# Kernel tuning notes

Measured on AMD Instinct MI355X. Metric: run time of the kernel, lower is better.

## Reference

```python
import jax, jax.numpy as jnp
import numpy as np

N, S, I, L, M = 4096, 8, 256, 512, 256


def setup_inputs() -> dict:
    key = jax.random.key(0)
    ks = jax.random.split(key, 13)
    sc_in = 1.0 / np.sqrt(I + L)
    sc_out = 1.0 / np.sqrt(L)
    return {
        "modulation": jax.random.normal(ks[0], (N, S * I), jnp.float32),
        "h0": jax.random.normal(ks[1], (N, S * L), jnp.float32),
        "c0": jax.random.normal(ks[2], (N, S * L), jnp.float32),
        "Wi": jax.random.normal(ks[3], (S, L, I + L), jnp.float32) * sc_in,
        "bi": jnp.full((S, L), -1.0, jnp.float32),  # init_input bias
        "Wf": jax.random.normal(ks[4], (S, L, I + L), jnp.float32) * sc_in,
        "bf": jnp.full((S, L), 1.0, jnp.float32),   # init_forget bias
        "Wg": jax.random.normal(ks[5], (S, L, I + L), jnp.float32) * sc_in,
        "bg": jnp.zeros((S, L), jnp.float32),
        "Wo": jax.random.normal(ks[6], (S, L, I + L), jnp.float32) * sc_in,
        "bo": jnp.zeros((S, L), jnp.float32),
        "Wy": jax.random.normal(ks[7], (S, M, L), jnp.float32) * sc_out,
        "by": jnp.zeros((S, M), jnp.float32),
    }


def reference(modulation, h0, c0, Wi, bi, Wf, bf, Wg, bg, Wo, bo, Wy, by):
    n = modulation.shape[0]
    x = modulation.reshape(n, S, I)          # [N,S,I]
    h = h0.reshape(n, S, L)                  # [N,S,L]
    c = c0.reshape(n, S, L)
    xh = jnp.concatenate([x, h], axis=-1)    # cat_groups: per-stream [x_s, h_s] -> [N,S,I+L]
    # grouped per-stream linear projections for the four gates
    i = jax.nn.sigmoid(jnp.einsum('nsd,sld->nsl', xh, Wi) + bi)
    f = jax.nn.sigmoid(jnp.einsum('nsd,sld->nsl', xh, Wf) + bf)
    g = jnp.tanh(jnp.einsum('nsd,sld->nsl', xh, Wg) + bg)
    o = jax.nn.sigmoid(jnp.einsum('nsd,sld->nsl', xh, Wo) + bo)
    c_new = f * c + i * g
    h_new = o * jnp.tanh(c_new)              # dropout p=0 -> identity
    y = jnp.einsum('nsl,sml->nsm', h_new, Wy) + by
    return y.reshape(n, S * M)
```

## Files before the change

### kernel.cpp

```cpp
#include <hip/hip_runtime.h>
#include <stdint.h>

#define S_ 8
#define N_ 4096
#define I_ 256
#define L_ 512
#define M_ 256
#define D_ 768
#define NT64 12

typedef __bf16 bf16x8 __attribute__((ext_vector_type(8)));
typedef float f32x4 __attribute__((ext_vector_type(4)));
typedef unsigned short ushort_t;

__device__ __forceinline__ unsigned short f2bf(float f) {
  union { float f; uint32_t u; } c; c.f = f;
  uint32_t u = c.u;
  uint32_t r = u + 0x7FFFu + ((u >> 16) & 1u);
  return (unsigned short)(r >> 16);
}

__device__ __forceinline__ float fsigmoid(float x) {
  return 1.0f / (1.0f + __expf(-x));
}
__device__ __forceinline__ float ftanh(float x) {
  float ax = fabsf(x);
  float e = __expf(-2.0f * ax);
  float t = (1.0f - e) / (1.0f + e);
  return copysignf(t, x);
}

#define GLD16(gsrc, ldst)                                                                  \
  __builtin_amdgcn_global_load_lds(                                                        \
      (const __attribute__((address_space(1))) uint32_t*)(uintptr_t)(gsrc),                \
      (__attribute__((address_space(3))) uint32_t*)(uintptr_t)(ldst), 16, 0, 0)

__global__ __launch_bounds__(256) void prep_kernel(
    const float* __restrict__ mod, const float* __restrict__ h0,
    const float* __restrict__ Wi, const float* __restrict__ Wf,
    const float* __restrict__ Wg, const float* __restrict__ Wo,
    const float* __restrict__ Wy, ushort_t* __restrict__ w4,
    ushort_t* __restrict__ wyb, ushort_t* __restrict__ xh) {
  const int y = blockIdx.y;
  int t = blockIdx.x * 256 + threadIdx.x;
  const int stride = gridDim.x * 256;
  if (y < 4) {
    const float* src = (y == 0) ? Wi : (y == 1) ? Wf : (y == 2) ? Wg : Wo;
    ushort_t* dst = w4 + (size_t)y * S_ * L_ * D_;
    const int n4 = S_ * L_ * D_ / 4;
    for (; t < n4; t += stride) {
      float4 v = ((const float4*)src)[t];
      ushort4 o;
      o.x = f2bf(v.x); o.y = f2bf(v.y); o.z = f2bf(v.z); o.w = f2bf(v.w);
      ((ushort4*)dst)[t] = o;
    }
  } else if (y == 4) {
    const int n4 = S_ * M_ * L_ / 4;
    for (; t < n4; t += stride) {
      float4 v = ((const float4*)Wy)[t];
      ushort4 o;
      o.x = f2bf(v.x); o.y = f2bf(v.y); o.z = f2bf(v.z); o.w = f2bf(v.w);
      ((ushort4*)wyb)[t] = o;
    }
  } else if (y == 5) {
    const int total = S_ * N_ * (I_ / 4);
    for (; t < total; t += stride) {
      int r = t >> 6, c = t & 63;
      int s = r >> 12, n = r & (N_ - 1);
      float4 v = *(const float4*)(mod + (size_t)n * (S_ * I_) + s * I_ + c * 4);
      ushort4 o;
      o.x = f2bf(v.x); o.y = f2bf(v.y); o.z = f2bf(v.z); o.w = f2bf(v.w);
      *(ushort4*)(xh + (size_t)r * D_ + c * 4) = o;
    }
  } else {
    const int total = S_ * N_ * (L_ / 4);
    for (; t < total; t += stride) {
      int r = t >> 7, c = t & 127;
      int s = r >> 12, n = r & (N_ - 1);
      float4 v = *(const float4*)(h0 + (size_t)n * (S_ * L_) + s * L_ + c * 4);
      ushort4 o;
      o.x = f2bf(v.x); o.y = f2bf(v.y); o.z = f2bf(v.z); o.w = f2bf(v.w);
      *(ushort4*)(xh + (size_t)r * D_ + I_ + c * 4) = o;
    }
  }
}

__global__ __launch_bounds__(1024, 4) void gates_kernel(
    const ushort_t* __restrict__ xh,
    const ushort_t* __restrict__ w4,
    const float* __restrict__ bi, const float* __restrict__ bff,
    const float* __restrict__ bg, const float* __restrict__ bo,
    const float* __restrict__ c0,
    ushort_t* __restrict__ hout)
{
  __shared__ __align__(16) ushort_t smem[65536];
  const int tid = threadIdx.x;
  const int lane = tid & 63;
  const int ln15 = lane & 15;
  const int ln4 = lane >> 4;
  const int w = tid >> 6;
  const int wm = w >> 2;
  const int wl = w & 3;

  const int bid = blockIdx.x;
  const int s = bid & 7;
  const int r = bid >> 3;
  const int n0 = (r >> 3) << 8;
  const int l0 = (r & 7) << 6;

  const size_t xh_base = (size_t)(s * N_ + n0) * D_;

  const ushort_t* aSrc[2];
  const ushort_t* bSrc[2];
  #pragma unroll
  for (int rd = 0; rd < 2; ++rd) {
    int slot = tid + (rd << 10);
    int row = slot >> 3;
    int cg = (slot & 7) ^ (row & 7);
    aSrc[rd] = xh + xh_base + (size_t)row * D_ + (cg << 3);
    int g = row >> 6, ll = row & 63;
    bSrc[rd] = w4 + ((size_t)((g * S_ + s) * L_) + l0 + ll) * D_ + (cg << 3);
  }

#define STAGE(base, tile) do {                                                          \
    const int k0_ = (tile) << 6;                                                        \
    GLD16(aSrc[0] + k0_, &smem[((base) + (w << 6)) * 8]);                               \
    GLD16(aSrc[1] + k0_, &smem[((base) + 1024 + (w << 6)) * 8]);                        \
    GLD16(bSrc[0] + k0_, &smem[((base) + 2048 + (w << 6)) * 8]);                        \
    GLD16(bSrc[1] + k0_, &smem[((base) + 3072 + (w << 6)) * 8]);                        \
  } while (0)

  f32x4 acc[4][4];
  #pragma unroll
  for (int i = 0; i < 4; ++i)
    #pragma unroll
    for (int j = 0; j < 4; ++j) {
      f32x4 z = {0.f, 0.f, 0.f, 0.f};
      acc[i][j] = z;
    }

  STAGE(0, 0);
  asm volatile("s_waitcnt vmcnt(0)" ::: "memory");
  __syncthreads();

  #pragma unroll 1
  for (int t = 0; t < NT64; ++t) {
    const int cur = (t & 1) << 12;
    if (t + 1 < NT64) STAGE(cur ^ 4096, t + 1);

    #pragma unroll
    for (int kk = 0; kk < 2; ++kk) {
      const int ch = (kk << 2) + ln4;
      bf16x8 a[4];
      #pragma unroll
      for (int rt = 0; rt < 4; ++rt) {
        int ra = (wm << 6) + (rt << 4) + ln15;
        a[rt] = *(const bf16x8*)&smem[(cur + (ra << 3) + (ch ^ (ra & 7))) * 8];
      }
      bf16x8 b[4];
      #pragma unroll
      for (int g = 0; g < 4; ++g) {
        int rB = (g << 6) + (wl << 4) + ln15;
        b[g] = *(const bf16x8*)&smem[(cur + 2048 + (rB << 3) + (ch ^ (rB & 7))) * 8];
      }
      #pragma unroll
      for (int rt = 0; rt < 4; ++rt)
        #pragma unroll
        for (int g = 0; g < 4; ++g)
          acc[rt][g] = __builtin_amdgcn_mfma_f32_16x16x32_bf16(a[rt], b[g], acc[rt][g], 0, 0, 0);
    }

    asm volatile("s_waitcnt vmcnt(0)" ::: "memory");
    __syncthreads();
  }

  const int l = l0 + (wl << 4) + ln15;
  const float vbi = bi[s * L_ + l];
  const float vbf = bff[s * L_ + l];
  const float vbg = bg[s * L_ + l];
  const float vbo = bo[s * L_ + l];
  #pragma unroll
  for (int rt = 0; rt < 4; ++rt) {
    #pragma unroll
    for (int j = 0; j < 4; ++j) {
      const int n = n0 + (wm << 6) + (rt << 4) + (ln4 << 2) + j;
      const float c0v = c0[(size_t)n * (S_ * L_) + s * L_ + l];
      const float iv = fsigmoid(acc[rt][0][j] + vbi);
      const float fv = fsigmoid(acc[rt][1][j] + vbf);
      const float gv = ftanh(acc[rt][2][j] + vbg);
      const float ov = fsigmoid(acc[rt][3][j] + vbo);
      const float cn = fv * c0v + iv * gv;
      const float hn = ov * ftanh(cn);
      hout[(size_t)(s * N_ + n) * L_ + l] = f2bf(hn);
    }
  }
#undef STAGE
}

__global__ __launch_bounds__(256, 2) void out_kernel(
    const ushort_t* __restrict__ h,
    const ushort_t* __restrict__ wy,
    const float* __restrict__ by,
    float* __restrict__ out)
{
  __shared__ __align__(16) ushort_t smem[1536 * 8];
  const int tid = threadIdx.x;
  const int lane = tid & 63;
  const int w = tid >> 6;
  const int n0 = blockIdx.x * 128;
  const int m0 = blockIdx.y * 64;
  const int s = blockIdx.z;

  f32x4 acc[2][4];
  #pragma unroll
  for (int rt = 0; rt < 2; ++rt)
    #pragma unroll
    for (int ct = 0; ct < 4; ++ct) {
      f32x4 z = {0.f, 0.f, 0.f, 0.f};
      acc[rt][ct] = z;
    }

  const size_t h_row0 = (size_t)(s * N_ + n0) * L_;

  for (int t = 0; t < L_ / 64; ++t) {
    const int k0 = t * 64;
    #pragma unroll
    for (int it = 0; it < 4; ++it) {
      int chunk = it * 256 + tid;
      int rr = chunk >> 3, c = chunk & 7;
      int cg = c ^ (rr & 7);
      const ushort_t* src = h + h_row0 + (size_t)rr * L_ + k0 + cg * 8;
      GLD16(src, &smem[(it * 256 + w * 64) * 8]);
    }
    #pragma unroll
    for (int it = 0; it < 2; ++it) {
      int chunk = it * 256 + tid;
      int rl = chunk >> 3, c = chunk & 7;
      int cg = c ^ (rl & 7);
      const ushort_t* src = wy + ((size_t)(s * M_ + m0 + rl)) * L_ + k0 + cg * 8;
      GLD16(src, &smem[(1024 + it * 256 + w * 64) * 8]);
    }
    __syncthreads();
    #pragma unroll
    for (int kk = 0; kk < 2; ++kk) {
      const int cc = kk * 4 + (lane >> 4);
      bf16x8 av[2];
      #pragma unroll
      for (int rt = 0; rt < 2; ++rt) {
        int rr = w * 32 + rt * 16 + (lane & 15);
        av[rt] = *(const bf16x8*)&smem[(rr * 8 + (cc ^ (rr & 7))) * 8];
      }
      #pragma unroll
      for (int ct = 0; ct < 4; ++ct) {
        int rl = ct * 16 + (lane & 15);
        bf16x8 b = *(const bf16x8*)&smem[(1024 + rl * 8 + (cc ^ (rl & 7))) * 8];
        acc[0][ct] = __builtin_amdgcn_mfma_f32_16x16x32_bf16(av[0], b, acc[0][ct], 0, 0, 0);
        acc[1][ct] = __builtin_amdgcn_mfma_f32_16x16x32_bf16(av[1], b, acc[1][ct], 0, 0, 0);
      }
    }
    __syncthreads();
  }

  #pragma unroll
  for (int ct = 0; ct < 4; ++ct) {
    const int m = m0 + ct * 16 + (lane & 15);
    const float vb = by[s * M_ + m];
    #pragma unroll
    for (int rt = 0; rt < 2; ++rt) {
      #pragma unroll
      for (int j = 0; j < 4; ++j) {
        const int n = n0 + w * 32 + rt * 16 + (lane >> 4) * 4 + j;
        out[(size_t)n * (S_ * M_) + s * M_ + m] = acc[rt][ct][j] + vb;
      }
    }
  }
}


extern "C" void kernel_launch(void* const* d_in, const int* in_sizes, int n_in,
                              void* d_out, int out_size, void* d_ws, size_t ws_size,
                              hipStream_t stream) {
  const float* mod = (const float*)d_in[0];
  const float* h0  = (const float*)d_in[1];
  const float* c0  = (const float*)d_in[2];
  const float* Wi  = (const float*)d_in[3];
  const float* bi  = (const float*)d_in[4];
  const float* Wf  = (const float*)d_in[5];
  const float* bf  = (const float*)d_in[6];
  const float* Wg  = (const float*)d_in[7];
  const float* bg  = (const float*)d_in[8];
  const float* Wo  = (const float*)d_in[9];
  const float* bo  = (const float*)d_in[10];
  const float* Wy  = (const float*)d_in[11];
  const float* by  = (const float*)d_in[12];
  float* out = (float*)d_out;

  ushort_t* ws = (ushort_t*)d_ws;
  ushort_t* xh   = ws;
  ushort_t* w4   = xh  + (size_t)S_ * N_ * D_;
  ushort_t* wyb  = w4  + (size_t)4 * S_ * L_ * D_;
  ushort_t* hbuf = wyb + (size_t)S_ * M_ * L_;

  prep_kernel<<<dim3(768, 7), 256, 0, stream>>>(mod, h0, Wi, Wf, Wg, Wo, Wy, w4, wyb, xh);
  gates_kernel<<<1024, 1024, 0, stream>>>(xh, w4, bi, bf, bg, bo, c0, hbuf);
  out_kernel<<<dim3(N_ / 128, M_ / 64, S_), 256, 0, stream>>>(hbuf, wyb, by, out);
}
```

Before: 197.8 us.

## Halve gates block threads, double per-wave tile, software-pipeline LDS reads and prefetch

The gates GEMM block drops from 1024 to 512 threads, so each wave now computes an 8x4 MFMA tile, twice the rows it handled before. Global loads are now prefetched two K-tiles ahead using partial vmcnt waits. The two K-halves of each tile have their LDS fragment reads double-buffered in registers so reads overlap MFMAs. The aim is to cut barrier/sync overhead and LDS traffic per MFMA and to hide global latency better, at the cost of more VGPRs/AGPRs and possibly lower occupancy.

```diff
diff --git a/kernel.cpp b/kernel.cpp
--- a/kernel.cpp
+++ b/kernel.cpp
@@ -85,7 +85,7 @@
   }
 }
 
-__global__ __launch_bounds__(1024, 4) void gates_kernel(
+__global__ __launch_bounds__(512, 2) void gates_kernel(
     const ushort_t* __restrict__ xh,
     const ushort_t* __restrict__ w4,
     const float* __restrict__ bi, const float* __restrict__ bff,
@@ -110,11 +110,11 @@
 
   const size_t xh_base = (size_t)(s * N_ + n0) * D_;
 
-  const ushort_t* aSrc[2];
-  const ushort_t* bSrc[2];
-  #pragma unroll
-  for (int rd = 0; rd < 2; ++rd) {
-    int slot = tid + (rd << 10);
+  const ushort_t* aSrc[4];
+  const ushort_t* bSrc[4];
+  #pragma unroll
+  for (int rd = 0; rd < 4; ++rd) {
+    int slot = tid + (rd << 9);
     int row = slot >> 3;
     int cg = (slot & 7) ^ (row & 7);
     aSrc[rd] = xh + xh_base + (size_t)row * D_ + (cg << 3);
@@ -122,56 +122,82 @@
     bSrc[rd] = w4 + ((size_t)((g * S_ + s) * L_) + l0 + ll) * D_ + (cg << 3);
   }
 
-#define STAGE(base, tile) do {                                                          \
+#define STAGE(bs, tile) do {                                                            \
     const int k0_ = (tile) << 6;                                                        \
-    GLD16(aSrc[0] + k0_, &smem[((base) + (w << 6)) * 8]);                               \
-    GLD16(aSrc[1] + k0_, &smem[((base) + 1024 + (w << 6)) * 8]);                        \
-    GLD16(bSrc[0] + k0_, &smem[((base) + 2048 + (w << 6)) * 8]);                        \
-    GLD16(bSrc[1] + k0_, &smem[((base) + 3072 + (w << 6)) * 8]);                        \
+    _Pragma("unroll")                                                                   \
+    for (int rd_ = 0; rd_ < 4; ++rd_) {                                                 \
+      GLD16(aSrc[rd_] + k0_, &smem[((bs) + (rd_ << 9) + (w << 6)) * 8]);                \
+      GLD16(bSrc[rd_] + k0_, &smem[((bs) + 2048 + (rd_ << 9) + (w << 6)) * 8]);         \
+    }                                                                                   \
   } while (0)
 
-  f32x4 acc[4][4];
-  #pragma unroll
-  for (int i = 0; i < 4; ++i)
+  const char* smemB = (const char*)smem;
+  const uint32_t chk0 = (uint32_t)((ln4 ^ (ln15 & 7)) << 4);
+  const uint32_t chk1 = (uint32_t)(((4 + ln4) ^ (ln15 & 7)) << 4);
+  const uint32_t aBase = (uint32_t)(((wm << 7) + ln15) << 7);
+  const uint32_t bBase = 32768u + (uint32_t)(((wl << 4) + ln15) << 7);
+  const uint32_t aK0 = aBase + chk0, aK1 = aBase + chk1;
+  const uint32_t bK0 = bBase + chk0, bK1 = bBase + chk1;
+
+#define READS(dstA, dstB, aK, bK, bufB) do {                                            \
+    const char* pA_ = smemB + ((aK) + (bufB));                                          \
+    const char* pB_ = smemB + ((bK) + (bufB));                                          \
+    _Pragma("unroll")                                                                   \
+    for (int rt_ = 0; rt_ < 8; ++rt_) dstA[rt_] = *(const bf16x8*)(pA_ + rt_ * 2048);   \
+    _Pragma("unroll")                                                                   \
+    for (int g_ = 0; g_ < 4; ++g_) dstB[g_] = *(const bf16x8*)(pB_ + g_ * 8192);        \
+  } while (0)
+
+#define MFMAS(aset, bset) do {                                                          \
+    _Pragma("unroll")                                                                   \
+    for (int rt_ = 0; rt_ < 8; ++rt_)                                                   \
+      _Pragma("unroll")                                                                 \
+      for (int g_ = 0; g_ < 4; ++g_)                                                    \
+        acc[rt_][g_] = __builtin_amdgcn_mfma_f32_16x16x32_bf16(                         \
+            aset[rt_], bset[g_], acc[rt_][g_], 0, 0, 0);                                \
+  } while (0)
+
+#define LGKM0() asm volatile("s_waitcnt lgkmcnt(0)")
+#define BAR() __builtin_amdgcn_s_barrier()
+
+  f32x4 acc[8][4];
+  #pragma unroll
+  for (int i = 0; i < 8; ++i)
     #pragma unroll
     for (int j = 0; j < 4; ++j) {
       f32x4 z = {0.f, 0.f, 0.f, 0.f};
       acc[i][j] = z;
     }
 
+  bf16x8 a0[8], b0[4], a1[8], b1[4];
+
   STAGE(0, 0);
-  asm volatile("s_waitcnt vmcnt(0)" ::: "memory");
-  __syncthreads();
+  STAGE(4096, 1);
+  asm volatile("s_waitcnt vmcnt(8)" ::: "memory");
+  BAR();
+  READS(a0, b0, aK0, bK0, 0u);
+  LGKM0();
 
   #pragma unroll 1
   for (int t = 0; t < NT64; ++t) {
-    const int cur = (t & 1) << 12;
-    if (t + 1 < NT64) STAGE(cur ^ 4096, t + 1);
-
-    #pragma unroll
-    for (int kk = 0; kk < 2; ++kk) {
-      const int ch = (kk << 2) + ln4;
-      bf16x8 a[4];
-      #pragma unroll
-      for (int rt = 0; rt < 4; ++rt) {
-        int ra = (wm << 6) + (rt << 4) + ln15;
-        a[rt] = *(const bf16x8*)&smem[(cur + (ra << 3) + (ch ^ (ra & 7))) * 8];
-      }
-      bf16x8 b[4];
-      #pragma unroll
-      for (int g = 0; g < 4; ++g) {
-        int rB = (g << 6) + (wl << 4) + ln15;
-        b[g] = *(const bf16x8*)&smem[(cur + 2048 + (rB << 3) + (ch ^ (rB & 7))) * 8];
-      }
-      #pragma unroll
-      for (int rt = 0; rt < 4; ++rt)
-        #pragma unroll
-        for (int g = 0; g < 4; ++g)
-          acc[rt][g] = __builtin_amdgcn_mfma_f32_16x16x32_bf16(a[rt], b[g], acc[rt][g], 0, 0, 0);
-    }
-
-    asm volatile("s_waitcnt vmcnt(0)" ::: "memory");
-    __syncthreads();
+    const uint32_t curB = (uint32_t)(t & 1) << 16;
+    const uint32_t nxtB = curB ^ 65536u;
+    const int bsCur = (t & 1) << 12;
+
+    READS(a1, b1, aK1, bK1, curB);
+    MFMAS(a0, b0);
+    LGKM0();
+    BAR();
+    if (t + 2 < NT64) STAGE(bsCur, t + 2);
+    if (t < NT64 - 2) {
+      asm volatile("s_waitcnt vmcnt(8)" ::: "memory");
+    } else {
+      asm volatile("s_waitcnt vmcnt(0)" ::: "memory");
+    }
+    BAR();
+    if (t + 1 < NT64) READS(a0, b0, aK0, bK0, nxtB);
+    MFMAS(a1, b1);
+    LGKM0();
   }
 
   const int l = l0 + (wl << 4) + ln15;
@@ -180,10 +206,10 @@
   const float vbg = bg[s * L_ + l];
   const float vbo = bo[s * L_ + l];
   #pragma unroll
-  for (int rt = 0; rt < 4; ++rt) {
+  for (int rt = 0; rt < 8; ++rt) {
     #pragma unroll
     for (int j = 0; j < 4; ++j) {
-      const int n = n0 + (wm << 6) + (rt << 4) + (ln4 << 2) + j;
+      const int n = n0 + (wm << 7) + (rt << 4) + (ln4 << 2) + j;
       const float c0v = c0[(size_t)n * (S_ * L_) + s * L_ + l];
       const float iv = fsigmoid(acc[rt][0][j] + vbi);
       const float fv = fsigmoid(acc[rt][1][j] + vbf);
@@ -195,6 +221,10 @@
     }
   }
 #undef STAGE
+#undef READS
+#undef MFMAS
+#undef LGKM0
+#undef BAR
 }
 
 __global__ __launch_bounds__(256, 2) void out_kernel(
@@ -302,6 +332,6 @@
   ushort_t* hbuf = wyb + (size_t)S_ * M_ * L_;
 
   prep_kernel<<<dim3(768, 7), 256, 0, stream>>>(mod, h0, Wi, Wf, Wg, Wo, Wy, w4, wyb, xh);
-  gates_kernel<<<1024, 1024, 0, stream>>>(xh, w4, bi, bf, bg, bo, c0, hbuf);
+  gates_kernel<<<1024, 512, 0, stream>>>(xh, w4, bi, bf, bg, bo, c0, hbuf);
   out_kernel<<<dim3(N_ / 128, M_ / 64, S_), 256, 0, stream>>>(hbuf, wyb, by, out);
 }
```

Measured after the change: 209.7 us. 6.0% more time.

## Halve gates kernel tile to 128 rows with 32-wide K steps and 512 threads

Applied to the files above, without the earlier changes.

The gates GEMM block now covers 128 batch rows instead of 256 and runs 512 threads instead of 1024. It steps K in chunks of 32 instead of 64, which halves shared memory per block and doubles the grid to 2048 blocks. The LDS swizzle and address math are reworked into precomputed byte offsets for the narrower tile. This is meant to raise occupancy and spread work across more blocks, at the cost of less operand reuse per block and twice as many barrier iterations.

```diff
diff --git a/kernel.cpp b/kernel.cpp
--- a/kernel.cpp
+++ b/kernel.cpp
@@ -7,7 +7,7 @@
 #define L_ 512
 #define M_ 256
 #define D_ 768
-#define NT64 12
+#define NT32 24
 
 typedef __bf16 bf16x8 __attribute__((ext_vector_type(8)));
 typedef float f32x4 __attribute__((ext_vector_type(4)));
@@ -85,7 +85,7 @@
   }
 }
 
-__global__ __launch_bounds__(1024, 4) void gates_kernel(
+__global__ __launch_bounds__(512, 4) void gates_kernel(
     const ushort_t* __restrict__ xh,
     const ushort_t* __restrict__ w4,
     const float* __restrict__ bi, const float* __restrict__ bff,
@@ -93,7 +93,7 @@
     const float* __restrict__ c0,
     ushort_t* __restrict__ hout)
 {
-  __shared__ __align__(16) ushort_t smem[65536];
+  __shared__ __align__(16) ushort_t smem[32768];
   const int tid = threadIdx.x;
   const int lane = tid & 63;
   const int ln15 = lane & 15;
@@ -105,30 +105,39 @@
   const int bid = blockIdx.x;
   const int s = bid & 7;
   const int r = bid >> 3;
-  const int n0 = (r >> 3) << 8;
+  const int n0 = (r >> 3) << 7;
   const int l0 = (r & 7) << 6;
 
   const size_t xh_base = (size_t)(s * N_ + n0) * D_;
 
-  const ushort_t* aSrc[2];
+  const ushort_t* aSrc;
+  {
+    int slot = tid;
+    int sr = slot >> 3, ch0 = (slot & 7) ^ (sr & 7);
+    int row = (sr << 1) | (ch0 >> 2), c = ch0 & 3;
+    aSrc = xh + xh_base + (size_t)row * D_ + (c << 3);
+  }
   const ushort_t* bSrc[2];
   #pragma unroll
   for (int rd = 0; rd < 2; ++rd) {
-    int slot = tid + (rd << 10);
-    int row = slot >> 3;
-    int cg = (slot & 7) ^ (row & 7);
-    aSrc[rd] = xh + xh_base + (size_t)row * D_ + (cg << 3);
+    int slot = tid + (rd << 9);
+    int sr = slot >> 3, ch0 = (slot & 7) ^ (sr & 7);
+    int row = (sr << 1) | (ch0 >> 2), c = ch0 & 3;
     int g = row >> 6, ll = row & 63;
-    bSrc[rd] = w4 + ((size_t)((g * S_ + s) * L_) + l0 + ll) * D_ + (cg << 3);
-  }
-
-#define STAGE(base, tile) do {                                                          \
-    const int k0_ = (tile) << 6;                                                        \
-    GLD16(aSrc[0] + k0_, &smem[((base) + (w << 6)) * 8]);                               \
-    GLD16(aSrc[1] + k0_, &smem[((base) + 1024 + (w << 6)) * 8]);                        \
-    GLD16(bSrc[0] + k0_, &smem[((base) + 2048 + (w << 6)) * 8]);                        \
-    GLD16(bSrc[1] + k0_, &smem[((base) + 3072 + (w << 6)) * 8]);                        \
+    bSrc[rd] = w4 + ((size_t)((g * S_ + s) * L_) + l0 + ll) * D_ + (c << 3);
+  }
+
+#define STAGE(bs, tile) do {                                                            \
+    const int k0_ = (tile) << 5;                                                        \
+    GLD16(aSrc + k0_, &smem[((bs) + (w << 6)) * 8]);                                    \
+    GLD16(bSrc[0] + k0_, &smem[((bs) + 512 + (w << 6)) * 8]);                           \
+    GLD16(bSrc[1] + k0_, &smem[((bs) + 1024 + (w << 6)) * 8]);                          \
   } while (0)
+
+  const char* smemB = (const char*)smem;
+  const uint32_t chk = (uint32_t)(((((ln15 & 1) << 2) | ln4) ^ (ln15 >> 1)) << 4);
+  const uint32_t aK = (uint32_t)((wm << 12) + ((ln15 >> 1) << 7)) + chk;
+  const uint32_t bK = 8192u + (uint32_t)((wl << 10) + ((ln15 >> 1) << 7)) + chk;
 
   f32x4 acc[4][4];
   #pragma unroll
@@ -144,31 +153,23 @@
   __syncthreads();
 
   #pragma unroll 1
-  for (int t = 0; t < NT64; ++t) {
-    const int cur = (t & 1) << 12;
-    if (t + 1 < NT64) STAGE(cur ^ 4096, t + 1);
-
-    #pragma unroll
-    for (int kk = 0; kk < 2; ++kk) {
-      const int ch = (kk << 2) + ln4;
-      bf16x8 a[4];
+  for (int t = 0; t < NT32; ++t) {
+    const int bsCur = (t & 1) << 11;
+    const uint32_t curB = (uint32_t)(t & 1) << 15;
+    if (t + 1 < NT32) STAGE(bsCur ^ 2048, t + 1);
+
+    const char* pA = smemB + (aK + curB);
+    const char* pB = smemB + (bK + curB);
+    bf16x8 a[4], b[4];
+    #pragma unroll
+    for (int rt = 0; rt < 4; ++rt) a[rt] = *(const bf16x8*)(pA + rt * 1024);
+    #pragma unroll
+    for (int g = 0; g < 4; ++g) b[g] = *(const bf16x8*)(pB + g * 4096);
+    #pragma unroll
+    for (int rt = 0; rt < 4; ++rt)
       #pragma unroll
-      for (int rt = 0; rt < 4; ++rt) {
-        int ra = (wm << 6) + (rt << 4) + ln15;
-        a[rt] = *(const bf16x8*)&smem[(cur + (ra << 3) + (ch ^ (ra & 7))) * 8];
-      }
-      bf16x8 b[4];
-      #pragma unroll
-      for (int g = 0; g < 4; ++g) {
-        int rB = (g << 6) + (wl << 4) + ln15;
-        b[g] = *(const bf16x8*)&smem[(cur + 2048 + (rB << 3) + (ch ^ (rB & 7))) * 8];
-      }
-      #pragma unroll
-      for (int rt = 0; rt < 4; ++rt)
-        #pragma unroll
-        for (int g = 0; g < 4; ++g)
-          acc[rt][g] = __builtin_amdgcn_mfma_f32_16x16x32_bf16(a[rt], b[g], acc[rt][g], 0, 0, 0);
-    }
+      for (int g = 0; g < 4; ++g)
+        acc[rt][g] = __builtin_amdgcn_mfma_f32_16x16x32_bf16(a[rt], b[g], acc[rt][g], 0, 0, 0);
 
     asm volatile("s_waitcnt vmcnt(0)" ::: "memory");
     __syncthreads();
@@ -302,6 +303,6 @@
   ushort_t* hbuf = wyb + (size_t)S_ * M_ * L_;
 
   prep_kernel<<<dim3(768, 7), 256, 0, stream>>>(mod, h0, Wi, Wf, Wg, Wo, Wy, w4, wyb, xh);
-  gates_kernel<<<1024, 1024, 0, stream>>>(xh, w4, bi, bf, bg, bo, c0, hbuf);
+  gates_kernel<<<2048, 512, 0, stream>>>(xh, w4, bi, bf, bg, bo, c0, hbuf);
   out_kernel<<<dim3(N_ / 128, M_ / 64, S_), 256, 0, stream>>>(hbuf, wyb, by, out);
 }
```

After: 214.2 us. 1.08x slower.
